# Optimization experiments

Hardware: AMD Instinct MI355X
Metric: run time of the kernel (lower is better)

Reference implementation:

```python
import jax, jax.numpy as jnp
import numpy as np

L, B, T, C = 4, 4, 2048, 1024
FFN = 4 * C
STD = 0.02
EPS = 1e-5
NEG_INF = -1e38


def setup_inputs() -> dict:
    key = jax.random.key(0)
    ks = jax.random.split(key, 18)
    n = lambda k, shape, s=STD: jax.random.normal(k, shape, jnp.float32) * s
    u = lambda k, shape: jax.random.uniform(k, shape, jnp.float32)
    return {
        "x": jax.random.normal(ks[0], (B, T, C), jnp.float32),
        "ln1_w": jnp.ones((L, C), jnp.float32),
        "tm_mix_k": u(ks[1], (L, 1, 1, C)),
        "tm_mix_v": u(ks[2], (L, 1, 1, C)),
        "tm_mix_r": u(ks[3], (L, 1, 1, C)),
        "tm_k_w": n(ks[4], (L, C, C)),
        "tm_v_w": n(ks[5], (L, C, C)),
        "tm_r_w": n(ks[6], (L, C, C)),
        "tm_o_w": n(ks[7], (L, C, C)),
        # time_decay in [-5, 1] like RWKV decay_speed init; w = -exp(time_decay)
        "time_decay": u(ks[8], (L, C)) * 6.0 - 5.0,
        "time_first": jnp.log(0.3).astype(jnp.float32) + 0.5 * jax.random.normal(ks[9], (L, C), jnp.float32),
        "ln2_w": jnp.ones((L, C), jnp.float32),
        "cm_mix_k": u(ks[10], (L, 1, 1, C)),
        "cm_mix_r": u(ks[11], (L, 1, 1, C)),
        "cm_k_w": n(ks[12], (L, FFN, C)),
        "cm_v_w": n(ks[13], (L, C, FFN)),
        "cm_r_w": n(ks[14], (L, C, C)),
        "lnf_w": jnp.ones((C,), jnp.float32),
    }


def layer_norm(x, w):
    mu = jnp.mean(x, axis=-1, keepdims=True)
    var = jnp.mean(jnp.square(x - mu), axis=-1, keepdims=True)
    return (x - mu) * jax.lax.rsqrt(var + EPS) * w


def time_shift(x):
    # ZeroPad2d((0,0,1,-1)): shift sequence right by one, zero at t=0
    return jnp.pad(x, ((0, 0), (1, 0), (0, 0)))[:, :-1]


def wkv_scan(k, v, time_decay, time_first):
    # k, v: [B, T, C]; numerically-stabilized linear WKV recurrence over T
    w = -jnp.exp(time_decay)  # [C]
    u = time_first            # [C]
    zeros = jnp.zeros(k.shape[::2], k.dtype)  # [B, C]

    def step(carry, kv):
        num, den, mx = carry
        kt, vt = kv
        max_out = jnp.maximum(mx, kt + u)
        e1 = jnp.exp(mx - max_out)
        e2 = jnp.exp(kt + u - max_out)
        out = (e1 * num + e2 * vt) / (e1 * den + e2)
        max_st = jnp.maximum(mx + w, kt)
        e1 = jnp.exp(mx + w - max_st)
        e2 = jnp.exp(kt - max_st)
        return (e1 * num + e2 * vt, e1 * den + e2, max_st), out

    init = (zeros, zeros, jnp.full_like(zeros, NEG_INF))
    _, out = jax.lax.scan(step, init, (k.swapaxes(0, 1), v.swapaxes(0, 1)))
    return out.swapaxes(0, 1)  # [B, T, C]


def reference(x, ln1_w, tm_mix_k, tm_mix_v, tm_mix_r, tm_k_w, tm_v_w, tm_r_w, tm_o_w,
              time_decay, time_first, ln2_w, cm_mix_k, cm_mix_r, cm_k_w, cm_v_w, cm_r_w, lnf_w):
    n_layer = ln1_w.shape[0]
    for l in range(n_layer):
        # --- TimeMixing ---
        h = layer_norm(x, ln1_w[l])
        prev = time_shift(h)
        k = jnp.einsum('btc,oc->bto', h * tm_mix_k[l] + prev * (1 - tm_mix_k[l]), tm_k_w[l])
        v = jnp.einsum('btc,oc->bto', h * tm_mix_v[l] + prev * (1 - tm_mix_v[l]), tm_v_w[l])
        r = jax.nn.sigmoid(jnp.einsum('btc,oc->bto', h * tm_mix_r[l] + prev * (1 - tm_mix_r[l]), tm_r_w[l]))
        wkv = wkv_scan(k, v, time_decay[l], time_first[l])
        x = x + jnp.einsum('btc,oc->bto', r * wkv, tm_o_w[l])
        # --- ChannelMixing ---
        h = layer_norm(x, ln2_w[l])
        prev = time_shift(h)
        kk = jnp.einsum('btc,fc->btf', h * cm_mix_k[l] + prev * (1 - cm_mix_k[l]), cm_k_w[l])  # [B,T,4C]
        vv = jnp.einsum('btf,of->bto', jnp.square(jax.nn.relu(kk)), cm_v_w[l])
        rr = jax.nn.sigmoid(jnp.einsum('btc,oc->bto', h * cm_mix_r[l] + prev * (1 - cm_mix_r[l]), cm_r_w[l]))
        x = x + rr * vv
    return layer_norm(x, lnf_w)
```

## Files before the change

### kernel.cpp

```cpp
#include <hip/hip_runtime.h>
#include <hip/hip_bf16.h>


#define LNUM 4
#define BSZ  4
#define TSZ  2048
#define CSZ  1024
#define FFND 4096
#define MROWS (BSZ*TSZ)
#define EPSF 1e-5f

typedef __hip_bfloat16 bf16;
typedef __bf16 bf16x8 __attribute__((ext_vector_type(8)));
typedef float f32x4 __attribute__((ext_vector_type(4)));

#define BM 128
#define BK 64

#define SCK  64
#define SLEN (TSZ/SCK)

__device__ __forceinline__ void async_copy16(const void* g, void* l) {
    __builtin_amdgcn_global_load_lds((const __attribute__((address_space(1))) void*)g,
                                     (__attribute__((address_space(3))) void*)l, 16, 0, 0);
}

template<int MODE, int TBN>
__launch_bounds__(256)
__global__ void gemm_bt(const bf16* __restrict__ A, const bf16* __restrict__ Bw,
                        void* __restrict__ outp, const bf16* __restrict__ aux,
                        int K, int LDK, int N)
{
    constexpr int MT  = (TBN == 128) ? 4 : 2;
    constexpr int NBI = TBN / 32;
    __shared__ __align__(16) __bf16 sA[BM*BK];
    __shared__ __align__(16) __bf16 sB[TBN*BK];
    const int tid  = threadIdx.x;
    const int lane = tid & 63;
    const int wid  = tid >> 6;
    const int wmB  = (TBN == 128) ? (wid >> 1) * 64 : wid * 32;
    const int wnB  = (TBN == 128) ? (wid & 1) * 64 : 0;
    const size_t bm0 = (size_t)blockIdx.x * BM;
    const size_t bn0 = (size_t)blockIdx.y * TBN;

    const int lrow8 = lane >> 3;
    const int cbg   = (lane & 7) ^ lrow8;

    const bf16* pA[4]; const bf16* pB[NBI];
#pragma unroll
    for (int i = 0; i < 4; ++i)
        pA[i] = A + (bm0 + (i*4 + wid)*8 + lrow8) * (size_t)LDK + cbg*8;
#pragma unroll
    for (int i = 0; i < NBI; ++i)
        pB[i] = Bw + (bn0 + (i*4 + wid)*8 + lrow8) * (size_t)LDK + cbg*8;

    f32x4 acc[MT][4];
#pragma unroll
    for (int a = 0; a < MT; ++a)
#pragma unroll
        for (int b = 0; b < 4; ++b) acc[a][b] = (f32x4){0.f,0.f,0.f,0.f};

    const int q   = lane >> 4;
    const int rlo = lane & 15;

    const int ktiles = K / BK;
    for (int kt = 0; kt < ktiles; ++kt) {
#pragma unroll
        for (int i = 0; i < 4; ++i) {
            async_copy16(pA[i], &sA[(i*4 + wid)*8*BK]);
            pA[i] += BK;
        }
#pragma unroll
        for (int i = 0; i < NBI; ++i) {
            async_copy16(pB[i], &sB[(i*4 + wid)*8*BK]);
            pB[i] += BK;
        }
        __syncthreads();
#pragma unroll
        for (int ks = 0; ks < 2; ++ks) {
            bf16x8 aF[MT], bF[4];
#pragma unroll
            for (int mt = 0; mt < MT; ++mt) {
                const int r  = wmB + mt*16 + rlo;
                const int cb = (ks*4 + q) ^ (r & 7);
                aF[mt] = *(const bf16x8*)&sA[r*BK + cb*8];
            }
#pragma unroll
            for (int nt = 0; nt < 4; ++nt) {
                const int r  = wnB + nt*16 + rlo;
                const int cb = (ks*4 + q) ^ (r & 7);
                bF[nt] = *(const bf16x8*)&sB[r*BK + cb*8];
            }
#pragma unroll
            for (int mt = 0; mt < MT; ++mt)
#pragma unroll
                for (int nt = 0; nt < 4; ++nt)
                    acc[mt][nt] = __builtin_amdgcn_mfma_f32_16x16x32_bf16(
                        aF[mt], bF[nt], acc[mt][nt], 0, 0, 0);
        }
        __syncthreads();
    }

#pragma unroll
    for (int mt = 0; mt < MT; ++mt) {
#pragma unroll
        for (int nt = 0; nt < 4; ++nt) {
            const size_t col = bn0 + wnB + nt*16 + rlo;
#pragma unroll
            for (int i = 0; i < 4; ++i) {
                const size_t row = bm0 + wmB + mt*16 + q*4 + i;
                const size_t idx = row * (size_t)N + col;
                const float v = acc[mt][nt][i];
                if (MODE == 2) {
                    ((float*)outp)[idx] += v;
                } else if (MODE == 6) {
                    ((float*)outp)[idx] = ((const float*)aux)[idx] + v;
                } else {
                    ((float*)outp)[idx] += (float)aux[idx] * v;
                }
            }
        }
    }
}

__launch_bounds__(256)
__global__ void gemm_kvr(const bf16* __restrict__ A0, const bf16* __restrict__ A1,
                         const bf16* __restrict__ A2,
                         const bf16* __restrict__ W0, const bf16* __restrict__ W1,
                         const bf16* __restrict__ W2,
                         bf16* __restrict__ O0, bf16* __restrict__ O1,
                         bf16* __restrict__ O2)
{
    constexpr int MT = 4, NBI = 4, K = CSZ, N = CSZ;
    const int z = blockIdx.z;
    const bf16* A  = (z == 0) ? A0 : (z == 1) ? A1 : A2;
    const bf16* Bw = (z == 0) ? W0 : (z == 1) ? W1 : W2;
    bf16* outp     = (z == 0) ? O0 : (z == 1) ? O1 : O2;

    __shared__ __align__(16) __bf16 sA[BM*BK];
    __shared__ __align__(16) __bf16 sB[128*BK];
    const int tid  = threadIdx.x;
    const int lane = tid & 63;
    const int wid  = tid >> 6;
    const int wmB  = (wid >> 1) * 64;
    const int wnB  = (wid & 1) * 64;
    const size_t bm0 = (size_t)blockIdx.x * BM;
    const size_t bn0 = (size_t)blockIdx.y * 128;

    const int lrow8 = lane >> 3;
    const int cbg   = (lane & 7) ^ lrow8;

    const bf16* pA[4]; const bf16* pB[NBI];
#pragma unroll
    for (int i = 0; i < 4; ++i)
        pA[i] = A + (bm0 + (i*4 + wid)*8 + lrow8) * (size_t)K + cbg*8;
#pragma unroll
    for (int i = 0; i < NBI; ++i)
        pB[i] = Bw + (bn0 + (i*4 + wid)*8 + lrow8) * (size_t)K + cbg*8;

    f32x4 acc[MT][4];
#pragma unroll
    for (int a = 0; a < MT; ++a)
#pragma unroll
        for (int b = 0; b < 4; ++b) acc[a][b] = (f32x4){0.f,0.f,0.f,0.f};

    const int q   = lane >> 4;
    const int rlo = lane & 15;

    for (int kt = 0; kt < K/BK; ++kt) {
#pragma unroll
        for (int i = 0; i < 4; ++i) {
            async_copy16(pA[i], &sA[(i*4 + wid)*8*BK]);
            pA[i] += BK;
        }
#pragma unroll
        for (int i = 0; i < NBI; ++i) {
            async_copy16(pB[i], &sB[(i*4 + wid)*8*BK]);
            pB[i] += BK;
        }
        __syncthreads();
#pragma unroll
        for (int ks = 0; ks < 2; ++ks) {
            bf16x8 aF[MT], bF[4];
#pragma unroll
            for (int mt = 0; mt < MT; ++mt) {
                const int r  = wmB + mt*16 + rlo;
                const int cb = (ks*4 + q) ^ (r & 7);
                aF[mt] = *(const bf16x8*)&sA[r*BK + cb*8];
            }
#pragma unroll
            for (int nt = 0; nt < 4; ++nt) {
                const int r  = wnB + nt*16 + rlo;
                const int cb = (ks*4 + q) ^ (r & 7);
                bF[nt] = *(const bf16x8*)&sB[r*BK + cb*8];
            }
#pragma unroll
            for (int mt = 0; mt < MT; ++mt)
#pragma unroll
                for (int nt = 0; nt < 4; ++nt)
                    acc[mt][nt] = __builtin_amdgcn_mfma_f32_16x16x32_bf16(
                        aF[mt], bF[nt], acc[mt][nt], 0, 0, 0);
        }
        __syncthreads();
    }

#pragma unroll
    for (int mt = 0; mt < MT; ++mt) {
#pragma unroll
        for (int nt = 0; nt < 4; ++nt) {
            const size_t col = bn0 + wnB + nt*16 + rlo;
#pragma unroll
            for (int i = 0; i < 4; ++i) {
                const size_t row = bm0 + wmB + mt*16 + q*4 + i;
                float v = acc[mt][nt][i];
                if (z == 2) v = 1.f/(1.f+__expf(-v));
                ((bf16*)outp)[row * (size_t)N + col] = __float2bfloat16(v);
            }
        }
    }
}

__launch_bounds__(256)
__global__ void gemm_cmkr(const bf16* __restrict__ Ak, const bf16* __restrict__ Ar,
                          const bf16* __restrict__ Wk, const bf16* __restrict__ Wr,
                          bf16* __restrict__ Ok, bf16* __restrict__ Or)
{
    constexpr int MT = 4, NBI = 4, K = CSZ;
    const bool isk = (blockIdx.y < FFND/128);
    const bf16* A  = isk ? Ak : Ar;
    const bf16* Bw = isk ? Wk : Wr;
    bf16* outp     = isk ? Ok : Or;
    const int N    = isk ? FFND : CSZ;
    const size_t bn0 = (size_t)(isk ? blockIdx.y : blockIdx.y - FFND/128) * 128;

    __shared__ __align__(16) __bf16 sA[BM*BK];
    __shared__ __align__(16) __bf16 sB[128*BK];
    const int tid  = threadIdx.x;
    const int lane = tid & 63;
    const int wid  = tid >> 6;
    const int wmB  = (wid >> 1) * 64;
    const int wnB  = (wid & 1) * 64;
    const size_t bm0 = (size_t)blockIdx.x * BM;

    const int lrow8 = lane >> 3;
    const int cbg   = (lane & 7) ^ lrow8;

    const bf16* pA[4]; const bf16* pB[NBI];
#pragma unroll
    for (int i = 0; i < 4; ++i)
        pA[i] = A + (bm0 + (i*4 + wid)*8 + lrow8) * (size_t)K + cbg*8;
#pragma unroll
    for (int i = 0; i < NBI; ++i)
        pB[i] = Bw + (bn0 + (i*4 + wid)*8 + lrow8) * (size_t)K + cbg*8;

    f32x4 acc[MT][4];
#pragma unroll
    for (int a = 0; a < MT; ++a)
#pragma unroll
        for (int b = 0; b < 4; ++b) acc[a][b] = (f32x4){0.f,0.f,0.f,0.f};

    const int q   = lane >> 4;
    const int rlo = lane & 15;

    for (int kt = 0; kt < K/BK; ++kt) {
#pragma unroll
        for (int i = 0; i < 4; ++i) {
            async_copy16(pA[i], &sA[(i*4 + wid)*8*BK]);
            pA[i] += BK;
        }
#pragma unroll
        for (int i = 0; i < NBI; ++i) {
            async_copy16(pB[i], &sB[(i*4 + wid)*8*BK]);
            pB[i] += BK;
        }
        __syncthreads();
#pragma unroll
        for (int ks = 0; ks < 2; ++ks) {
            bf16x8 aF[MT], bF[4];
#pragma unroll
            for (int mt = 0; mt < MT; ++mt) {
                const int r  = wmB + mt*16 + rlo;
                const int cb = (ks*4 + q) ^ (r & 7);
                aF[mt] = *(const bf16x8*)&sA[r*BK + cb*8];
            }
#pragma unroll
            for (int nt = 0; nt < 4; ++nt) {
                const int r  = wnB + nt*16 + rlo;
                const int cb = (ks*4 + q) ^ (r & 7);
                bF[nt] = *(const bf16x8*)&sB[r*BK + cb*8];
            }
#pragma unroll
            for (int mt = 0; mt < MT; ++mt)
#pragma unroll
                for (int nt = 0; nt < 4; ++nt)
                    acc[mt][nt] = __builtin_amdgcn_mfma_f32_16x16x32_bf16(
                        aF[mt], bF[nt], acc[mt][nt], 0, 0, 0);
        }
        __syncthreads();
    }

#pragma unroll
    for (int mt = 0; mt < MT; ++mt) {
#pragma unroll
        for (int nt = 0; nt < 4; ++nt) {
            const size_t col = bn0 + wnB + nt*16 + rlo;
#pragma unroll
            for (int i = 0; i < 4; ++i) {
                const size_t row = bm0 + wmB + mt*16 + q*4 + i;
                const float v = acc[mt][nt][i];
                float o;
                if (isk) { const float t = fmaxf(v, 0.f); o = t*t; }
                else     { o = 1.f/(1.f+__expf(-v)); }
                ((bf16*)outp)[row * (size_t)N + col] = __float2bfloat16(o);
            }
        }
    }
}

template<int NOUT>
__launch_bounds__(256)
__global__ void ln_mix_kernel(const float* __restrict__ x, const float* __restrict__ lnw,
                              const float* __restrict__ mka, const float* __restrict__ mva,
                              const float* __restrict__ mra,
                              bf16* __restrict__ ok, bf16* __restrict__ ov, bf16* __restrict__ orr)
{
    const int bt  = blockIdx.x;
    const int t   = bt % TSZ;
    const int tid = threadIdx.x;
    const float4 xc = ((const float4*)(x + (size_t)bt*CSZ))[tid];
    float4 xp = {0.f,0.f,0.f,0.f};
    const bool hasp = (t != 0);
    if (hasp) xp = ((const float4*)(x + (size_t)(bt-1)*CSZ))[tid];

    float s0 = xc.x+xc.y+xc.z+xc.w;
    float s1 = xc.x*xc.x+xc.y*xc.y+xc.z*xc.z+xc.w*xc.w;
    float s2 = xp.x+xp.y+xp.z+xp.w;
    float s3 = xp.x*xp.x+xp.y*xp.y+xp.z*xp.z+xp.w*xp.w;
#pragma unroll
    for (int off = 32; off > 0; off >>= 1) {
        s0 += __shfl_down(s0, off); s1 += __shfl_down(s1, off);
        s2 += __shfl_down(s2, off); s3 += __shfl_down(s3, off);
    }
    __shared__ float red[4][4];
    if ((tid & 63) == 0) { const int wq = tid >> 6;
        red[wq][0]=s0; red[wq][1]=s1; red[wq][2]=s2; red[wq][3]=s3; }
    __syncthreads();
    s0 = red[0][0]+red[1][0]+red[2][0]+red[3][0];
    s1 = red[0][1]+red[1][1]+red[2][1]+red[3][1];
    s2 = red[0][2]+red[1][2]+red[2][2]+red[3][2];
    s3 = red[0][3]+red[1][3]+red[2][3]+red[3][3];

    const float inv = 1.f/CSZ;
    const float muC = s0*inv;
    const float rsC = rsqrtf(s1*inv - muC*muC + EPSF);
    const float muP = s2*inv;
    const float rsP = rsqrtf(s3*inv - muP*muP + EPSF);

    const int c4 = tid*4;
    const float4 lw = ((const float4*)lnw)[tid];
    const float4 mk = ((const float4*)mka)[tid];
    const float4 mv = (NOUT >= 2) ? ((const float4*)mva)[tid] : lw;
    const float4 mr = (NOUT >= 3) ? ((const float4*)mra)[tid] : lw;

    float hcv[4] = {(xc.x-muC)*rsC*lw.x, (xc.y-muC)*rsC*lw.y,
                    (xc.z-muC)*rsC*lw.z, (xc.w-muC)*rsC*lw.w};
    float hpv[4];
    if (hasp) {
        hpv[0]=(xp.x-muP)*rsP*lw.x; hpv[1]=(xp.y-muP)*rsP*lw.y;
        hpv[2]=(xp.z-muP)*rsP*lw.z; hpv[3]=(xp.w-muP)*rsP*lw.w;
    } else { hpv[0]=hpv[1]=hpv[2]=hpv[3]=0.f; }
    const float mkv[4]={mk.x,mk.y,mk.z,mk.w};
    const float mvv[4]={mv.x,mv.y,mv.z,mv.w};
    const float mrv[4]={mr.x,mr.y,mr.z,mr.w};

    __align__(8) bf16 o0[4], o1[4], o2[4];
#pragma unroll
    for (int j = 0; j < 4; ++j) {
        o0[j] = __float2bfloat16(hcv[j]*mkv[j] + hpv[j]*(1.f-mkv[j]));
        if (NOUT >= 2) o1[j] = __float2bfloat16(hcv[j]*mvv[j] + hpv[j]*(1.f-mvv[j]));
        if (NOUT >= 3) o2[j] = __float2bfloat16(hcv[j]*mrv[j] + hpv[j]*(1.f-mrv[j]));
    }
    *(uint2*)(ok + (size_t)bt*CSZ + c4) = *(const uint2*)o0;
    if (NOUT >= 2) *(uint2*)(ov  + (size_t)bt*CSZ + c4) = *(const uint2*)o1;
    if (NOUT >= 3) *(uint2*)(orr + (size_t)bt*CSZ + c4) = *(const uint2*)o2;
}

__launch_bounds__(256)
__global__ void wkv_sum_kernel(const bf16* __restrict__ kb, const bf16* __restrict__ vb,
                               const float* __restrict__ td,
                               float* __restrict__ sN, float* __restrict__ sD,
                               float* __restrict__ sM)
{
    const int j  = blockIdx.x;
    const int b  = blockIdx.y >> 2;
    const int cg = blockIdx.y & 3;
    const int c  = cg*256 + threadIdx.x;
    const float w = -__expf(td[c]);

    size_t idx = ((size_t)b*TSZ + j*SLEN)*CSZ + c;
    float num = 0.f, den = 0.f, mx = -1e38f;
    float kt = (float)kb[idx], vt = (float)vb[idx];
    for (int t = 0; t < SLEN; ++t) {
        float kn = 0.f, vn = 0.f;
        if (t + 1 < SLEN) {
            kn = (float)kb[idx + CSZ]; vn = (float)vb[idx + CSZ];
        }
        const float ms = fmaxf(mx + w, kt);
        const float p1 = __expf(mx + w - ms);
        const float p2 = __expf(kt - ms);
        num = p1*num + p2*vt; den = p1*den + p2; mx = ms;
        idx += CSZ; kt = kn; vt = vn;
    }
    const size_t sidx = ((size_t)b*SCK + j)*CSZ + c;
    sN[sidx] = num; sD[sidx] = den; sM[sidx] = mx;
}

__launch_bounds__(256)
__global__ void wkv_out_kernel(const bf16* __restrict__ kb, const bf16* __restrict__ vb,
                               const bf16* __restrict__ rb,
                               const float* __restrict__ td, const float* __restrict__ tf,
                               const float* __restrict__ sN, const float* __restrict__ sD,
                               const float* __restrict__ sM,
                               bf16* __restrict__ outb)
{
    const int j  = blockIdx.x;
    const int b  = blockIdx.y >> 2;
    const int cg = blockIdx.y & 3;
    const int c  = cg*256 + threadIdx.x;
    const float w = -__expf(td[c]);
    const float u = tf[c];
    const float wL = w * (float)SLEN;

    float num = 0.f, den = 0.f, mx = -1e38f;
    size_t pidx = (size_t)b*SCK*CSZ + c;
    for (int jj = 0; jj < j; ++jj) {
        const float nl = sN[pidx], dl = sD[pidx], ml = sM[pidx];
        const float mi = mx + wL;
        const float mo = fmaxf(mi, ml);
        const float e1 = __expf(mi - mo);
        const float e2 = __expf(ml - mo);
        num = e1*num + e2*nl; den = e1*den + e2*dl; mx = mo;
        pidx += CSZ;
    }

    size_t idx = ((size_t)b*TSZ + j*SLEN)*CSZ + c;
    float kt = (float)kb[idx], vt = (float)vb[idx], rt = (float)rb[idx];
    for (int t = 0; t < SLEN; ++t) {
        float kn = 0.f, vn = 0.f, rn = 0.f;
        if (t + 1 < SLEN) {
            kn = (float)kb[idx + CSZ]; vn = (float)vb[idx + CSZ]; rn = (float)rb[idx + CSZ];
        }
        const float ku = kt + u;
        const float mo = fmaxf(mx, ku);
        const float e1 = __expf(mx - mo);
        const float e2 = __expf(ku - mo);
        const float outv = (e1*num + e2*vt) / (e1*den + e2);
        const float ms = fmaxf(mx + w, kt);
        const float p1 = __expf(mx + w - ms);
        const float p2 = __expf(kt - ms);
        num = p1*num + p2*vt; den = p1*den + p2; mx = ms;
        outb[idx] = __float2bfloat16(rt * outv);
        idx += CSZ; kt = kn; vt = vn; rt = rn;
    }
}

__launch_bounds__(256)
__global__ void final_ln_kernel(const float* __restrict__ x, const float* __restrict__ lnw,
                                float* __restrict__ out)
{
    const int bt  = blockIdx.x;
    const int tid = threadIdx.x;
    const float4 xc = ((const float4*)(x + (size_t)bt*CSZ))[tid];
    float s0 = xc.x+xc.y+xc.z+xc.w;
    float s1 = xc.x*xc.x+xc.y*xc.y+xc.z*xc.z+xc.w*xc.w;
#pragma unroll
    for (int off = 32; off > 0; off >>= 1) {
        s0 += __shfl_down(s0, off); s1 += __shfl_down(s1, off);
    }
    __shared__ float red[4][2];
    if ((tid & 63) == 0) { red[tid>>6][0] = s0; red[tid>>6][1] = s1; }
    __syncthreads();
    s0 = red[0][0]+red[1][0]+red[2][0]+red[3][0];
    s1 = red[0][1]+red[1][1]+red[2][1]+red[3][1];
    const float inv = 1.f/CSZ;
    const float mu = s0*inv;
    const float rs = rsqrtf(s1*inv - mu*mu + EPSF);
    const float4 lw = ((const float4*)lnw)[tid];
    float4 o;
    o.x = (xc.x-mu)*rs*lw.x; o.y = (xc.y-mu)*rs*lw.y;
    o.z = (xc.z-mu)*rs*lw.z; o.w = (xc.w-mu)*rs*lw.w;
    ((float4*)(out + (size_t)bt*CSZ))[tid] = o;
}

#define N4_CC (CSZ*CSZ/4)
#define N4_FC (FFND*CSZ/4)
__global__ void cvt_weights_kernel(const float* __restrict__ tk, const float* __restrict__ tv,
                                   const float* __restrict__ tr, const float* __restrict__ to,
                                   const float* __restrict__ ck, const float* __restrict__ cv,
                                   const float* __restrict__ cr,
                                   bf16* __restrict__ wk, bf16* __restrict__ wv,
                                   bf16* __restrict__ wr, bf16* __restrict__ wo,
                                   bf16* __restrict__ wck, bf16* __restrict__ wcv,
                                   bf16* __restrict__ wcr)
{
    int i = blockIdx.x * 256 + threadIdx.x;
    const float* s; bf16* d;
    if      (i < 1*N4_CC)          { s = tk; d = wk;  }
    else if (i < 2*N4_CC)          { s = tv; d = wv;  i -= 1*N4_CC; }
    else if (i < 3*N4_CC)          { s = tr; d = wr;  i -= 2*N4_CC; }
    else if (i < 4*N4_CC)          { s = to; d = wo;  i -= 3*N4_CC; }
    else if (i < 4*N4_CC+N4_FC)    { s = ck; d = wck; i -= 4*N4_CC; }
    else if (i < 4*N4_CC+2*N4_FC)  { s = cv; d = wcv; i -= 4*N4_CC+N4_FC; }
    else                           { s = cr; d = wcr; i -= 4*N4_CC+2*N4_FC; }
    const float4 f = ((const float4*)s)[i];
    __align__(8) bf16 o[4] = {__float2bfloat16(f.x), __float2bfloat16(f.y),
                              __float2bfloat16(f.z), __float2bfloat16(f.w)};
    ((uint2*)d)[i] = *(const uint2*)o;
}
#define CVT_TOTAL4 (4*N4_CC + 2*N4_FC + N4_CC)

static constexpr size_t SZ_XF32 = (size_t)MROWS*CSZ*4;
static constexpr size_t SZ_ABF  = (size_t)MROWS*CSZ*2;
static constexpr size_t OFF_X   = 0;
static constexpr size_t OFF_XK  = OFF_X  + SZ_XF32;
static constexpr size_t OFF_XV  = OFF_XK + SZ_ABF;
static constexpr size_t OFF_XR  = OFF_XV + SZ_ABF;
static constexpr size_t OFF_K   = OFF_XR + SZ_ABF;
static constexpr size_t OFF_V   = OFF_K  + SZ_ABF;
static constexpr size_t OFF_R   = OFF_V  + SZ_ABF;
static constexpr size_t OFF_KK  = OFF_R  + SZ_ABF;
static constexpr size_t OFF_W   = OFF_KK + (size_t)MROWS*FFND*2;
static constexpr size_t OFF_WK  = OFF_W;
static constexpr size_t OFF_WV  = OFF_WK + (size_t)CSZ*CSZ*2;
static constexpr size_t OFF_WR  = OFF_WV + (size_t)CSZ*CSZ*2;
static constexpr size_t OFF_WO  = OFF_WR + (size_t)CSZ*CSZ*2;
static constexpr size_t OFF_WCK = OFF_WO + (size_t)CSZ*CSZ*2;
static constexpr size_t OFF_WCV = OFF_WCK + (size_t)FFND*CSZ*2;
static constexpr size_t OFF_WCR = OFF_WCV + (size_t)CSZ*FFND*2;

static constexpr size_t SZ_SUM  = (size_t)BSZ*SCK*CSZ*4;

extern "C" void kernel_launch(void* const* d_in, const int* in_sizes, int n_in,
                              void* d_out, int out_size, void* d_ws, size_t ws_size,
                              hipStream_t stream)
{
    const float* xin   = (const float*)d_in[0];
    const float* ln1w  = (const float*)d_in[1];
    const float* tmixk = (const float*)d_in[2];
    const float* tmixv = (const float*)d_in[3];
    const float* tmixr = (const float*)d_in[4];
    const float* tkw   = (const float*)d_in[5];
    const float* tvw   = (const float*)d_in[6];
    const float* trw   = (const float*)d_in[7];
    const float* tow   = (const float*)d_in[8];
    const float* tdec  = (const float*)d_in[9];
    const float* tfst  = (const float*)d_in[10];
    const float* ln2w  = (const float*)d_in[11];
    const float* cmixk = (const float*)d_in[12];
    const float* cmixr = (const float*)d_in[13];
    const float* ckw   = (const float*)d_in[14];
    const float* cvw   = (const float*)d_in[15];
    const float* crw   = (const float*)d_in[16];
    const float* lnfw  = (const float*)d_in[17];

    char* ws = (char*)d_ws;
    float* xres = (float*)(ws + OFF_X);
    bf16* xk  = (bf16*)(ws + OFF_XK);
    bf16* xv  = (bf16*)(ws + OFF_XV);
    bf16* xr  = (bf16*)(ws + OFF_XR);
    bf16* kb  = (bf16*)(ws + OFF_K);
    bf16* vb  = (bf16*)(ws + OFF_V);
    bf16* rb  = (bf16*)(ws + OFF_R);
    bf16* kkb = (bf16*)(ws + OFF_KK);
    bf16* rwkv = xk;
    bf16* rr  = (bf16*)(ws + OFF_K);
    float* sN  = (float*)(ws + OFF_KK);
    float* sD  = (float*)(ws + OFF_KK + SZ_SUM);
    float* sM  = (float*)(ws + OFF_KK + 2*SZ_SUM);
    bf16* wk  = (bf16*)(ws + OFF_WK);
    bf16* wv  = (bf16*)(ws + OFF_WV);
    bf16* wr  = (bf16*)(ws + OFF_WR);
    bf16* wo  = (bf16*)(ws + OFF_WO);
    bf16* wck = (bf16*)(ws + OFF_WCK);
    bf16* wcv = (bf16*)(ws + OFF_WCV);
    bf16* wcr = (bf16*)(ws + OFF_WCR);

    const dim3 blk(256);
    const dim3 gKVR(MROWS/BM, CSZ/128, 3);
    const dim3 gC64(MROWS/BM, CSZ/64);
    const dim3 gCMKR(MROWS/BM, FFND/128 + CSZ/128);
    const dim3 gScan(SCK, BSZ*4);

    for (int l = 0; l < LNUM; ++l) {
        const size_t oC  = (size_t)l*CSZ;
        const size_t oCC = (size_t)l*CSZ*CSZ;
        const size_t oFC = (size_t)l*FFND*CSZ;
        cvt_weights_kernel<<<CVT_TOTAL4/256, blk, 0, stream>>>(
            tkw + oCC, tvw + oCC, trw + oCC, tow + oCC,
            ckw + oFC, cvw + oFC, crw + oCC,
            wk, wv, wr, wo, wck, wcv, wcr);

        ln_mix_kernel<3><<<MROWS, blk, 0, stream>>>(l == 0 ? xin : xres, ln1w + oC,
            tmixk + oC, tmixv + oC, tmixr + oC, xk, xv, xr);
        gemm_kvr<<<gKVR, blk, 0, stream>>>(xk, xv, xr, wk, wv, wr, kb, vb, rb);
        wkv_sum_kernel<<<gScan, blk, 0, stream>>>(kb, vb, tdec + oC, sN, sD, sM);
        wkv_out_kernel<<<gScan, blk, 0, stream>>>(kb, vb, rb, tdec + oC, tfst + oC,
            sN, sD, sM, rwkv);
        if (l == 0) {
            gemm_bt<6,64><<<gC64, blk, 0, stream>>>(rwkv, wo, xres,
                (const bf16*)xin, CSZ, CSZ, CSZ);
        } else {
            gemm_bt<2,64><<<gC64, blk, 0, stream>>>(rwkv, wo, xres, nullptr,
                CSZ, CSZ, CSZ);
        }

        ln_mix_kernel<2><<<MROWS, blk, 0, stream>>>(xres, ln2w + oC,
            cmixk + oC, cmixr + oC, nullptr, xk, xv, nullptr);
        gemm_cmkr<<<gCMKR, blk, 0, stream>>>(xk, xv, wck, wcr, kkb, rr);
        gemm_bt<5,64><<<gC64, blk, 0, stream>>>(kkb, wcv, xres, rr,
            FFND, FFND, CSZ);
    }
    final_ln_kernel<<<MROWS, blk, 0, stream>>>(xres, lnfw, (float*)d_out);
}
```

Measured before the change: 1.721 ms.

## Use 256x256 double-buffered pipelined GEMM for channel-mix key projection

Replaces the combined channel-mix key/receptance GEMM with a dedicated 512-thread, 256x256-tile kernel for the key projection. It double-buffers LDS, issues async global-to-LDS loads for the next K tile between MFMA phases using explicit vmcnt waits and barriers, and raises wave priority around MFMA bursts. The receptance projection now runs as a separate launch of the existing 64-wide GEMM with a new sigmoid-to-bf16 epilogue mode. This aims to raise MFMA utilization and data reuse on the largest GEMM, at the cost of an extra launch and higher register and LDS pressure.

```diff
diff --git a/kernel.cpp b/kernel.cpp
--- a/kernel.cpp
+++ b/kernel.cpp
@@ -23,6 +23,162 @@
 __device__ __forceinline__ void async_copy16(const void* g, void* l) {
     __builtin_amdgcn_global_load_lds((const __attribute__((address_space(1))) void*)g,
                                      (__attribute__((address_space(3))) void*)l, 16, 0, 0);
+}
+
+#define VM4  asm volatile("s_waitcnt vmcnt(4)" ::: "memory")
+#define VM0  asm volatile("s_waitcnt vmcnt(0)" ::: "memory")
+#define FEN  asm volatile("" ::: "memory")
+#define BARR __builtin_amdgcn_s_barrier()
+
+#define KT8 (CSZ/BK)
+__launch_bounds__(512, 2)
+__global__ void gemm_cmk8(const bf16* __restrict__ A, const bf16* __restrict__ Bw,
+                          bf16* __restrict__ outp)
+{
+    __shared__ __align__(16) __bf16 sT[2][2][2][8192];
+    const int tid  = threadIdx.x;
+    const int lane = tid & 63;
+    const int wid  = tid >> 6;
+    const int wr   = wid >> 2;
+    const int wc   = wid & 3;
+    const size_t bm0 = (size_t)blockIdx.x * 256;
+    const size_t bn0 = (size_t)blockIdx.y * 256;
+    const int q    = lane >> 4;
+    const int rlo  = lane & 15;
+    const int ss8  = (q ^ ((rlo >> 1) & 3)) * 8;
+
+    const int rl = lane >> 2;
+    const int sl = lane & 3;
+    const int r0 = wid*32 + rl;
+    const int r1 = wid*32 + 16 + rl;
+    const int c0 = sl ^ ((r0 >> 1) & 3);
+    const int c1 = sl ^ ((r1 >> 1) & 3);
+    const int ldsm0 = (wid*2 + 0) * 512;
+    const int ldsm1 = (wid*2 + 1) * 512;
+
+    const bf16* gA00 = A  + (bm0 + r0)*(size_t)CSZ +  0 + c0*8;
+    const bf16* gA01 = A  + (bm0 + r1)*(size_t)CSZ +  0 + c1*8;
+    const bf16* gA10 = A  + (bm0 + r0)*(size_t)CSZ + 32 + c0*8;
+    const bf16* gA11 = A  + (bm0 + r1)*(size_t)CSZ + 32 + c1*8;
+    const bf16* gB00 = Bw + (bn0 + r0)*(size_t)CSZ +  0 + c0*8;
+    const bf16* gB01 = Bw + (bn0 + r1)*(size_t)CSZ +  0 + c1*8;
+    const bf16* gB10 = Bw + (bn0 + r0)*(size_t)CSZ + 32 + c0*8;
+    const bf16* gB11 = Bw + (bn0 + r1)*(size_t)CSZ + 32 + c1*8;
+
+#define RD_A(bufi, ks, mt) (*(const bf16x8*)&sT[bufi][0][ks][(wr*128 + (mt)*16 + rlo)*32 + ss8])
+#define RD_B(bufi, ks, nt) (*(const bf16x8*)&sT[bufi][1][ks][(wc*64  + (nt)*16 + rlo)*32 + ss8])
+
+    f32x4 acc[8][4];
+#pragma unroll
+    for (int a = 0; a < 8; ++a)
+#pragma unroll
+        for (int b = 0; b < 4; ++b) acc[a][b] = (f32x4){0.f,0.f,0.f,0.f};
+
+    async_copy16(gA00, &sT[0][0][0][ldsm0]); async_copy16(gA01, &sT[0][0][0][ldsm1]);
+    async_copy16(gB00, &sT[0][1][0][ldsm0]); async_copy16(gB01, &sT[0][1][0][ldsm1]);
+    async_copy16(gA10, &sT[0][0][1][ldsm0]); async_copy16(gA11, &sT[0][0][1][ldsm1]);
+    async_copy16(gB10, &sT[0][1][1][ldsm0]); async_copy16(gB11, &sT[0][1][1][ldsm1]);
+
+    for (int kt = 0; kt < KT8; ++kt) {
+        const int buf  = kt & 1;
+        const int nb   = buf ^ 1;
+        const bool more = (kt + 1 < KT8);
+        const size_t ko = (size_t)(kt + 1) * BK;
+        bf16x8 aF[4], bF[4];
+
+        if (more) VM4; else VM0;
+        BARR;
+#pragma unroll
+        for (int mt = 0; mt < 4; ++mt) aF[mt] = RD_A(buf, 0, mt);
+#pragma unroll
+        for (int nt = 0; nt < 4; ++nt) bF[nt] = RD_B(buf, 0, nt);
+        if (more) {
+            async_copy16(gA00 + ko, &sT[nb][0][0][ldsm0]);
+            async_copy16(gA01 + ko, &sT[nb][0][0][ldsm1]);
+        }
+        __builtin_amdgcn_s_setprio(1);
+#pragma unroll
+        for (int mt = 0; mt < 4; ++mt)
+#pragma unroll
+            for (int nt = 0; nt < 4; ++nt)
+                acc[mt][nt] = __builtin_amdgcn_mfma_f32_16x16x32_bf16(
+                    aF[mt], bF[nt], acc[mt][nt], 0, 0, 0);
+        __builtin_amdgcn_s_setprio(0);
+        FEN; BARR;
+
+        if (more) VM4; else VM0;
+        BARR;
+#pragma unroll
+        for (int mt = 0; mt < 4; ++mt) aF[mt] = RD_A(buf, 0, mt + 4);
+        if (more) {
+            async_copy16(gB00 + ko, &sT[nb][1][0][ldsm0]);
+            async_copy16(gB01 + ko, &sT[nb][1][0][ldsm1]);
+        }
+        __builtin_amdgcn_s_setprio(1);
+#pragma unroll
+        for (int mt = 0; mt < 4; ++mt)
+#pragma unroll
+            for (int nt = 0; nt < 4; ++nt)
+                acc[mt+4][nt] = __builtin_amdgcn_mfma_f32_16x16x32_bf16(
+                    aF[mt], bF[nt], acc[mt+4][nt], 0, 0, 0);
+        __builtin_amdgcn_s_setprio(0);
+        FEN; BARR;
+
+        if (more) VM4; else VM0;
+        BARR;
+#pragma unroll
+        for (int mt = 0; mt < 4; ++mt) aF[mt] = RD_A(buf, 1, mt);
+#pragma unroll
+        for (int nt = 0; nt < 4; ++nt) bF[nt] = RD_B(buf, 1, nt);
+        if (more) {
+            async_copy16(gA10 + ko, &sT[nb][0][1][ldsm0]);
+            async_copy16(gA11 + ko, &sT[nb][0][1][ldsm1]);
+        }
+        __builtin_amdgcn_s_setprio(1);
+#pragma unroll
+        for (int mt = 0; mt < 4; ++mt)
+#pragma unroll
+            for (int nt = 0; nt < 4; ++nt)
+                acc[mt][nt] = __builtin_amdgcn_mfma_f32_16x16x32_bf16(
+                    aF[mt], bF[nt], acc[mt][nt], 0, 0, 0);
+        __builtin_amdgcn_s_setprio(0);
+        FEN; BARR;
+
+        if (more) VM4; else VM0;
+        BARR;
+#pragma unroll
+        for (int mt = 0; mt < 4; ++mt) aF[mt] = RD_A(buf, 1, mt + 4);
+        if (more) {
+            async_copy16(gB10 + ko, &sT[nb][1][1][ldsm0]);
+            async_copy16(gB11 + ko, &sT[nb][1][1][ldsm1]);
+        }
+        __builtin_amdgcn_s_setprio(1);
+#pragma unroll
+        for (int mt = 0; mt < 4; ++mt)
+#pragma unroll
+            for (int nt = 0; nt < 4; ++nt)
+                acc[mt+4][nt] = __builtin_amdgcn_mfma_f32_16x16x32_bf16(
+                    aF[mt], bF[nt], acc[mt+4][nt], 0, 0, 0);
+        __builtin_amdgcn_s_setprio(0);
+        FEN; BARR;
+    }
+
+#pragma unroll
+    for (int mt = 0; mt < 8; ++mt) {
+#pragma unroll
+        for (int nt = 0; nt < 4; ++nt) {
+            const size_t col = bn0 + wc*64 + nt*16 + rlo;
+#pragma unroll
+            for (int i = 0; i < 4; ++i) {
+                const size_t row = bm0 + wr*128 + mt*16 + q*4 + i;
+                const float v = acc[mt][nt][i];
+                const float t = fmaxf(v, 0.f);
+                outp[row * (size_t)FFND + col] = __float2bfloat16(t*t);
+            }
+        }
+    }
+#undef RD_A
+#undef RD_B
 }
 
 template<int MODE, int TBN>
@@ -113,6 +269,8 @@
                 const float v = acc[mt][nt][i];
                 if (MODE == 2) {
                     ((float*)outp)[idx] += v;
+                } else if (MODE == 4) {
+                    ((bf16*)outp)[idx] = __float2bfloat16(1.f/(1.f+__expf(-v)));
                 } else if (MODE == 6) {
                     ((float*)outp)[idx] = ((const float*)aux)[idx] + v;
                 } else {
@@ -215,103 +373,6 @@
                 float v = acc[mt][nt][i];
                 if (z == 2) v = 1.f/(1.f+__expf(-v));
                 ((bf16*)outp)[row * (size_t)N + col] = __float2bfloat16(v);
-            }
-        }
-    }
-}
-
-__launch_bounds__(256)
-__global__ void gemm_cmkr(const bf16* __restrict__ Ak, const bf16* __restrict__ Ar,
-                          const bf16* __restrict__ Wk, const bf16* __restrict__ Wr,
-                          bf16* __restrict__ Ok, bf16* __restrict__ Or)
-{
-    constexpr int MT = 4, NBI = 4, K = CSZ;
-    const bool isk = (blockIdx.y < FFND/128);
-    const bf16* A  = isk ? Ak : Ar;
-    const bf16* Bw = isk ? Wk : Wr;
-    bf16* outp     = isk ? Ok : Or;
-    const int N    = isk ? FFND : CSZ;
-    const size_t bn0 = (size_t)(isk ? blockIdx.y : blockIdx.y - FFND/128) * 128;
-
-    __shared__ __align__(16) __bf16 sA[BM*BK];
-    __shared__ __align__(16) __bf16 sB[128*BK];
-    const int tid  = threadIdx.x;
-    const int lane = tid & 63;
-    const int wid  = tid >> 6;
-    const int wmB  = (wid >> 1) * 64;
-    const int wnB  = (wid & 1) * 64;
-    const size_t bm0 = (size_t)blockIdx.x * BM;
-
-    const int lrow8 = lane >> 3;
-    const int cbg   = (lane & 7) ^ lrow8;
-
-    const bf16* pA[4]; const bf16* pB[NBI];
-#pragma unroll
-    for (int i = 0; i < 4; ++i)
-        pA[i] = A + (bm0 + (i*4 + wid)*8 + lrow8) * (size_t)K + cbg*8;
-#pragma unroll
-    for (int i = 0; i < NBI; ++i)
-        pB[i] = Bw + (bn0 + (i*4 + wid)*8 + lrow8) * (size_t)K + cbg*8;
-
-    f32x4 acc[MT][4];
-#pragma unroll
-    for (int a = 0; a < MT; ++a)
-#pragma unroll
-        for (int b = 0; b < 4; ++b) acc[a][b] = (f32x4){0.f,0.f,0.f,0.f};
-
-    const int q   = lane >> 4;
-    const int rlo = lane & 15;
-
-    for (int kt = 0; kt < K/BK; ++kt) {
-#pragma unroll
-        for (int i = 0; i < 4; ++i) {
-            async_copy16(pA[i], &sA[(i*4 + wid)*8*BK]);
-            pA[i] += BK;
-        }
-#pragma unroll
-        for (int i = 0; i < NBI; ++i) {
-            async_copy16(pB[i], &sB[(i*4 + wid)*8*BK]);
-            pB[i] += BK;
-        }
-        __syncthreads();
-#pragma unroll
-        for (int ks = 0; ks < 2; ++ks) {
-            bf16x8 aF[MT], bF[4];
-#pragma unroll
-            for (int mt = 0; mt < MT; ++mt) {
-                const int r  = wmB + mt*16 + rlo;
-                const int cb = (ks*4 + q) ^ (r & 7);
-                aF[mt] = *(const bf16x8*)&sA[r*BK + cb*8];
-            }
-#pragma unroll
-            for (int nt = 0; nt < 4; ++nt) {
-                const int r  = wnB + nt*16 + rlo;
-                const int cb = (ks*4 + q) ^ (r & 7);
-                bF[nt] = *(const bf16x8*)&sB[r*BK + cb*8];
-            }
-#pragma unroll
-            for (int mt = 0; mt < MT; ++mt)
-#pragma unroll
-                for (int nt = 0; nt < 4; ++nt)
-                    acc[mt][nt] = __builtin_amdgcn_mfma_f32_16x16x32_bf16(
-                        aF[mt], bF[nt], acc[mt][nt], 0, 0, 0);
-        }
-        __syncthreads();
-    }
-
-#pragma unroll
-    for (int mt = 0; mt < MT; ++mt) {
-#pragma unroll
-        for (int nt = 0; nt < 4; ++nt) {
-            const size_t col = bn0 + wnB + nt*16 + rlo;
-#pragma unroll
-            for (int i = 0; i < 4; ++i) {
-                const size_t row = bm0 + wmB + mt*16 + q*4 + i;
-                const float v = acc[mt][nt][i];
-                float o;
-                if (isk) { const float t = fmaxf(v, 0.f); o = t*t; }
-                else     { o = 1.f/(1.f+__expf(-v)); }
-                ((bf16*)outp)[row * (size_t)N + col] = __float2bfloat16(o);
             }
         }
     }
@@ -588,7 +649,7 @@
     const dim3 blk(256);
     const dim3 gKVR(MROWS/BM, CSZ/128, 3);
     const dim3 gC64(MROWS/BM, CSZ/64);
-    const dim3 gCMKR(MROWS/BM, FFND/128 + CSZ/128);
+    const dim3 gCMK8(MROWS/256, FFND/256);
     const dim3 gScan(SCK, BSZ*4);
 
     for (int l = 0; l < LNUM; ++l) {
@@ -616,7 +677,8 @@
 
         ln_mix_kernel<2><<<MROWS, blk, 0, stream>>>(xres, ln2w + oC,
             cmixk + oC, cmixr + oC, nullptr, xk, xv, nullptr);
-        gemm_cmkr<<<gCMKR, blk, 0, stream>>>(xk, xv, wck, wcr, kkb, rr);
+        gemm_cmk8<<<gCMK8, dim3(512), 0, stream>>>(xk, wck, kkb);
+        gemm_bt<4,64><<<gC64, blk, 0, stream>>>(xv, wcr, rr, nullptr, CSZ, CSZ, CSZ);
         gemm_bt<5,64><<<gC64, blk, 0, stream>>>(kkb, wcv, xres, rr,
             FFND, FFND, CSZ);
     }
```

Result: no change. 1.723 ms (+0.1%).

## Add dedicated 256x128-tile pipelined GEMM for channel-mix value projection

Applied to the files above, without the earlier changes.

Replaces the generic 128x64-tile gemm_bt used for the K=4096 channel-mix value GEMM with a specialized 512-thread kernel using 256x128 tiles, double-buffered LDS filled by async global-to-LDS loads, and fine-grained vmcnt waits interleaved with MFMA phases plus s_setprio. Larger tiles raise arithmetic intensity and cut global and LDS traffic per FLOP, and the interleaving aims to hide load latency behind compute. The generic kernel's MODE 5 path is removed. Risks include higher register pressure at two blocks per CU and fewer blocks (256) to fill the GPU.

```diff
diff --git a/kernel.cpp b/kernel.cpp
--- a/kernel.cpp
+++ b/kernel.cpp
@@ -23,6 +23,156 @@
 __device__ __forceinline__ void async_copy16(const void* g, void* l) {
     __builtin_amdgcn_global_load_lds((const __attribute__((address_space(1))) void*)g,
                                      (__attribute__((address_space(3))) void*)l, 16, 0, 0);
+}
+
+#define VM3  asm volatile("s_waitcnt vmcnt(3)" ::: "memory")
+#define VM0  asm volatile("s_waitcnt vmcnt(0)" ::: "memory")
+#define FEN  asm volatile("" ::: "memory")
+#define BARR __builtin_amdgcn_s_barrier()
+
+#define KTV (FFND/BK)
+__launch_bounds__(512, 2)
+__global__ void gemm_cmv8(const bf16* __restrict__ A, const bf16* __restrict__ Bw,
+                          float* __restrict__ outp, const bf16* __restrict__ aux)
+{
+    __shared__ __align__(16) __bf16 sA[2][2][8192];
+    __shared__ __align__(16) __bf16 sB[2][2][4096];
+    const int tid  = threadIdx.x;
+    const int lane = tid & 63;
+    const int wid  = tid >> 6;
+    const int wr   = wid >> 2;
+    const int wc   = wid & 3;
+    const size_t bm0 = (size_t)blockIdx.x * 256;
+    const size_t bn0 = (size_t)blockIdx.y * 128;
+    const int q    = lane >> 4;
+    const int rlo  = lane & 15;
+    const int ss8  = (q ^ ((rlo >> 1) & 3)) * 8;
+
+    const int rl4 = lane >> 2;
+    const int sl  = lane & 3;
+    const int c   = sl ^ ((rl4 >> 1) & 3);
+    const bf16* gA0 = A  + (bm0 + wid*16 + rl4)       * (size_t)FFND + c*8;
+    const bf16* gA1 = A  + (bm0 + 128 + wid*16 + rl4) * (size_t)FFND + c*8;
+    const bf16* gB0 = Bw + (bn0 + wid*16 + rl4)       * (size_t)FFND + c*8;
+    const int dA0 = (wid*16)*32;
+    const int dA1 = (128 + wid*16)*32;
+    const int dB  = (wid*16)*32;
+
+#define RDA(bufi, ks, mt) (*(const bf16x8*)&sA[bufi][ks][(wr*128 + (mt)*16 + rlo)*32 + ss8])
+#define RDB(bufi, ks, nt) (*(const bf16x8*)&sB[bufi][ks][(wc*32  + (nt)*16 + rlo)*32 + ss8])
+
+    f32x4 acc[8][2];
+#pragma unroll
+    for (int a = 0; a < 8; ++a)
+#pragma unroll
+        for (int b = 0; b < 2; ++b) acc[a][b] = (f32x4){0.f,0.f,0.f,0.f};
+
+    async_copy16(gA0,      &sA[0][0][dA0]);
+    async_copy16(gA1,      &sA[0][0][dA1]);
+    async_copy16(gB0,      &sB[0][0][dB]);
+    async_copy16(gA0 + 32, &sA[0][1][dA0]);
+    async_copy16(gA1 + 32, &sA[0][1][dA1]);
+    async_copy16(gB0 + 32, &sB[0][1][dB]);
+    VM3;
+    BARR;
+
+    for (int kt = 0; kt < KTV; ++kt) {
+        const int buf  = kt & 1;
+        const int nb   = buf ^ 1;
+        const bool more = (kt + 1 < KTV);
+        const size_t ko = (size_t)(kt + 1) * BK;
+        bf16x8 aF[4], bF[2];
+
+#pragma unroll
+        for (int mt = 0; mt < 4; ++mt) aF[mt] = RDA(buf, 0, mt);
+#pragma unroll
+        for (int nt = 0; nt < 2; ++nt) bF[nt] = RDB(buf, 0, nt);
+        if (more) {
+            async_copy16(gA0 + ko, &sA[nb][0][dA0]);
+            async_copy16(gA1 + ko, &sA[nb][0][dA1]);
+        }
+        BARR;
+        __builtin_amdgcn_s_setprio(1);
+#pragma unroll
+        for (int mt = 0; mt < 4; ++mt)
+#pragma unroll
+            for (int nt = 0; nt < 2; ++nt)
+                acc[mt][nt] = __builtin_amdgcn_mfma_f32_16x16x32_bf16(
+                    aF[mt], bF[nt], acc[mt][nt], 0, 0, 0);
+        __builtin_amdgcn_s_setprio(0);
+        FEN; BARR;
+
+#pragma unroll
+        for (int mt = 0; mt < 4; ++mt) aF[mt] = RDA(buf, 0, mt + 4);
+        if (more) {
+            async_copy16(gB0 + ko, &sB[nb][0][dB]);
+            VM3;
+        } else {
+            VM0;
+        }
+        BARR;
+        __builtin_amdgcn_s_setprio(1);
+#pragma unroll
+        for (int mt = 0; mt < 4; ++mt)
+#pragma unroll
+            for (int nt = 0; nt < 2; ++nt)
+                acc[mt+4][nt] = __builtin_amdgcn_mfma_f32_16x16x32_bf16(
+                    aF[mt], bF[nt], acc[mt+4][nt], 0, 0, 0);
+        __builtin_amdgcn_s_setprio(0);
+        FEN; BARR;
+
+#pragma unroll
+        for (int mt = 0; mt < 4; ++mt) aF[mt] = RDA(buf, 1, mt);
+#pragma unroll
+        for (int nt = 0; nt < 2; ++nt) bF[nt] = RDB(buf, 1, nt);
+        if (more) {
+            async_copy16(gA0 + ko + 32, &sA[nb][1][dA0]);
+            async_copy16(gA1 + ko + 32, &sA[nb][1][dA1]);
+        }
+        BARR;
+        __builtin_amdgcn_s_setprio(1);
+#pragma unroll
+        for (int mt = 0; mt < 4; ++mt)
+#pragma unroll
+            for (int nt = 0; nt < 2; ++nt)
+                acc[mt][nt] = __builtin_amdgcn_mfma_f32_16x16x32_bf16(
+                    aF[mt], bF[nt], acc[mt][nt], 0, 0, 0);
+        __builtin_amdgcn_s_setprio(0);
+        FEN; BARR;
+
+#pragma unroll
+        for (int mt = 0; mt < 4; ++mt) aF[mt] = RDA(buf, 1, mt + 4);
+        if (more) {
+            async_copy16(gB0 + ko + 32, &sB[nb][1][dB]);
+            VM3;
+        }
+        BARR;
+        __builtin_amdgcn_s_setprio(1);
+#pragma unroll
+        for (int mt = 0; mt < 4; ++mt)
+#pragma unroll
+            for (int nt = 0; nt < 2; ++nt)
+                acc[mt+4][nt] = __builtin_amdgcn_mfma_f32_16x16x32_bf16(
+                    aF[mt], bF[nt], acc[mt+4][nt], 0, 0, 0);
+        __builtin_amdgcn_s_setprio(0);
+        FEN; BARR;
+    }
+
+#pragma unroll
+    for (int mt = 0; mt < 8; ++mt) {
+#pragma unroll
+        for (int nt = 0; nt < 2; ++nt) {
+            const size_t col = bn0 + wc*32 + nt*16 + rlo;
+#pragma unroll
+            for (int i = 0; i < 4; ++i) {
+                const size_t row = bm0 + wr*128 + mt*16 + q*4 + i;
+                const size_t idx = row * (size_t)CSZ + col;
+                outp[idx] += (float)aux[idx] * acc[mt][nt][i];
+            }
+        }
+    }
+#undef RDA
+#undef RDB
 }
 
 template<int MODE, int TBN>
@@ -113,10 +263,8 @@
                 const float v = acc[mt][nt][i];
                 if (MODE == 2) {
                     ((float*)outp)[idx] += v;
-                } else if (MODE == 6) {
+                } else {
                     ((float*)outp)[idx] = ((const float*)aux)[idx] + v;
-                } else {
-                    ((float*)outp)[idx] += (float)aux[idx] * v;
                 }
             }
         }
@@ -589,6 +737,7 @@
     const dim3 gKVR(MROWS/BM, CSZ/128, 3);
     const dim3 gC64(MROWS/BM, CSZ/64);
     const dim3 gCMKR(MROWS/BM, FFND/128 + CSZ/128);
+    const dim3 gCMV8(MROWS/256, CSZ/128);
     const dim3 gScan(SCK, BSZ*4);
 
     for (int l = 0; l < LNUM; ++l) {
@@ -617,8 +766,7 @@
         ln_mix_kernel<2><<<MROWS, blk, 0, stream>>>(xres, ln2w + oC,
             cmixk + oC, cmixr + oC, nullptr, xk, xv, nullptr);
         gemm_cmkr<<<gCMKR, blk, 0, stream>>>(xk, xv, wck, wcr, kkb, rr);
-        gemm_bt<5,64><<<gC64, blk, 0, stream>>>(kkb, wcv, xres, rr,
-            FFND, FFND, CSZ);
+        gemm_cmv8<<<gCMV8, dim3(512), 0, stream>>>(kkb, wcv, xres, rr);
     }
     final_ln_kernel<<<MROWS, blk, 0, stream>>>(xres, lnfw, (float*)d_out);
 }
```

Result: no change. 1.728 ms (+0.4%).
